# Kernel tuning notes

Measured on AMD Instinct MI355X. Metric: run time of the kernel, lower is better.

## Reference

```python
import jax, jax.numpy as jnp
import numpy as np

B, D, L, H, E = 65536, 3, 64, 256, 8
N_HIDDEN_EXTRA = 2  # num_hidden_layers - 1


def setup_inputs() -> dict:
    key = jax.random.key(0)
    ks = jax.random.split(key, 12)
    s = 0.05
    return {
        "x": jax.random.normal(ks[0], (B, D), jnp.float32),
        "labels": jax.random.randint(ks[1], (B,), 0, E, jnp.int64),
        "eps": jax.random.normal(ks[2], (B, L), jnp.float32),
        "mu_table": jax.random.normal(ks[3], (E, L), jnp.float32) * s,
        "logvar_table": jax.random.normal(ks[4], (E, L), jnp.float32) * s,
        "W0": jax.random.normal(ks[5], (E, D + L, H), jnp.float32) * s,
        "b0": jnp.zeros((E, H), jnp.float32),
        "Wh": jax.random.normal(ks[6], (N_HIDDEN_EXTRA, E, H, H), jnp.float32) * s,
        "bh": jnp.zeros((N_HIDDEN_EXTRA, E, H), jnp.float32),
        "Wo": jax.random.normal(ks[7], (E, H, 1), jnp.float32) * s,
        "bo": jnp.zeros((E, 1), jnp.float32),
    }


def reference(x, labels, eps, mu_table, logvar_table, W0, b0, Wh, bh, Wo, bo):
    batch = x.shape[0]
    # encoder: embedding lookup by label
    mu = mu_table[labels]          # [B, L]
    logvar = logvar_table[labels]  # [B, L]
    z = mu + eps * jnp.exp(0.5 * logvar)
    kl = -0.5 * jnp.sum(1.0 + logvar - mu * mu - jnp.exp(logvar)) / batch
    x_in = jnp.concatenate([x, z], axis=1)  # [B, D+L]
    # MoE dispatch: run each expert on the full batch, mask by label
    out = jnp.zeros((batch, 1), x.dtype)
    n_exp = W0.shape[0]
    n_hid = Wh.shape[0]
    for e in range(n_exp):
        h = jax.nn.relu(x_in @ W0[e] + b0[e])
        for l in range(n_hid):
            h = jax.nn.relu(h @ Wh[l, e] + bh[l, e])
        oe = h @ Wo[e] + bo[e]  # [B, 1]
        out = out + jnp.where((labels == e)[:, None], oe, 0.0)
    return out, kl
```

## Files before the change

kernel.cpp:

```cpp
#include <hip/hip_runtime.h>
#include <hip/hip_bf16.h>
#include <stdint.h>

#define B_N 65536
#define L_N 64
#define E_N 8
#define SPB 64
#define MAXT (B_N/SPB + E_N)
#define NHB 256
#define NPW 608
typedef __attribute__((ext_vector_type(4))) float f32x4;
typedef __attribute__((ext_vector_type(8))) short short8;

__device__ __forceinline__ short f2bf(float f){
  union { float f; unsigned u; } v; v.f = f;
  unsigned r = (v.u + 0x7fffu + ((v.u >> 16) & 1u)) >> 16;
  return (short)r;
}

__global__ void k_prep(const int* __restrict__ labels,
                       const float* __restrict__ W0, const float* __restrict__ Wh,
                       unsigned* __restrict__ pcnt,
                       short* __restrict__ wf0, short* __restrict__ wf1){
  const int bid = blockIdx.x, tid = threadIdx.x;
  if(bid < NHB){
    __shared__ unsigned lc[8];
    if(tid < 8) lc[tid] = 0;
    __syncthreads();
    atomicAdd(&lc[labels[bid*256 + tid] & 7], 1u);
    __syncthreads();
    if(tid < 8) pcnt[bid*8 + tid] = lc[tid];
    return;
  }
  int uid = (bid - NHB) * 256 + tid;
  const int NU0 = 8*3*16*64;
  const int NU1 = 2*8*8*16*64;
  if(uid < NU0){
    int e = uid / 3072, r = uid % 3072;
    int s = r / 1024, r2 = r % 1024, t = r2 / 64, l = r2 % 64;
    int g = l >> 4, m = 16*t + (l & 15);
    short8 v;
    #pragma unroll
    for(int j=0;j<8;j++){
      int k = 32*s + 4*g + (j & 3) + 16*(j >> 2);
      float f = (k < 67) ? W0[(e*67 + k)*256 + m] : 0.f;
      v[j] = f2bf(f);
    }
    *(short8*)(wf0 + (size_t)uid * 8) = v;
  } else if(uid < NU0 + NU1){
    int u = uid - NU0;
    int lh = u / 65536, r = u % 65536;
    int e = r / 8192, r1 = r % 8192;
    int s = r1 / 1024, r2 = r1 % 1024, t = r2 / 64, l = r2 % 64;
    int g = l >> 4, m = 16*t + (l & 15);
    short8 v;
    #pragma unroll
    for(int j=0;j<8;j++){
      int k = 32*s + 4*g + (j & 3) + 16*(j >> 2);
      v[j] = f2bf(Wh[(((size_t)(lh*8 + e))*256 + k)*256 + m]);
    }
    *(short8*)(wf1 + (size_t)u * 8) = v;
  }
}

__global__ void k_scan(const unsigned* __restrict__ pcnt,
                       unsigned* __restrict__ sbase,
                       int* __restrict__ te, int* __restrict__ tb, int* __restrict__ tl,
                       const float* __restrict__ mu_t, const float* __restrict__ lv_t,
                       float* __restrict__ klout){
  __shared__ unsigned spc[NHB*8];
  __shared__ int off[9], ts[9];
  __shared__ unsigned cnt[8];
  __shared__ float fe[8];
  const int t = threadIdx.x;
  for(int i=t; i<NHB*8; i+=256) spc[i] = pcnt[i];
  __syncthreads();
  if(t < 8){
    unsigned run = 0;
    for(int b=0;b<NHB;b++){ unsigned v = spc[b*8+t]; spc[b*8+t] = run; run += v; }
    cnt[t] = run;
    float s = 0.f;
    for(int i=0;i<64;i++){
      float m = mu_t[t*64+i], l = lv_t[t*64+i];
      s += 1.f + l - m*m - expf(l);
    }
    fe[t] = s;
  }
  __syncthreads();
  if(t == 0){
    int o = 0, tt = 0;
    for(int e=0;e<8;e++){
      off[e] = o; ts[e] = tt;
      o += (int)cnt[e];
      tt += ((int)cnt[e] + SPB - 1) / SPB;
    }
    off[8] = o; ts[8] = tt;
    float kl = 0.f;
    for(int e=0;e<8;e++) kl += fe[e] * (float)cnt[e];
    klout[0] = -0.5f * kl / (float)B_N;
  }
  __syncthreads();
  for(int i=t; i<NHB*8; i+=256) sbase[i] = (unsigned)off[i & 7] + spc[i];
  for(int i=t; i<MAXT; i+=256){
    if(i < ts[8]){
      int e = 0;
      while(e < 7 && i >= ts[e+1]) e++;
      te[i] = e;
      tb[i] = off[e] + (i - ts[e]) * SPB;
      tl[i] = off[e] + (int)cnt[e];
    } else { te[i] = 0; tb[i] = 0; tl[i] = 0; }
  }
}

__global__ void k_scatter(const int* __restrict__ labels,
                          const unsigned* __restrict__ sbase,
                          int* __restrict__ perm){
  __shared__ unsigned lcnt[8];
  const int bid = blockIdx.x, tid = threadIdx.x;
  if(tid < 8) lcnt[tid] = 0;
  __syncthreads();
  int i = bid*256 + tid;
  int e = labels[i] & 7;
  unsigned r = atomicAdd(&lcnt[e], 1u);
  perm[sbase[bid*8 + e] + r] = i;
}

__global__ __launch_bounds__(256, 2) void k_mlp(
    const float* __restrict__ x, const float* __restrict__ eps,
    const float* __restrict__ mu_t, const float* __restrict__ lv_t,
    const float* __restrict__ b0, const float* __restrict__ bh,
    const float* __restrict__ Wo, const float* __restrict__ bo,
    const short* __restrict__ wf0, const short* __restrict__ wf1,
    const int* __restrict__ perm, const int* __restrict__ te,
    const int* __restrict__ tb, const int* __restrict__ tl,
    float* __restrict__ out)
{
  __shared__ __align__(16) short abuf[3][8192];
  __shared__ __align__(16) float bias_lds[3][256];
  __shared__ __align__(16) float wo_lds[256];

  const int tid  = threadIdx.x;
  const int w    = tid >> 6, lane = tid & 63;
  const int g    = lane >> 4, col = lane & 15;
  const int bid  = blockIdx.x;
  const int e = te[bid], base = tb[bid], lim = tl[bid];
  if(base >= lim) return;

  bias_lds[0][tid] = b0[e*256 + tid];
  bias_lds[1][tid] = bh[e*256 + tid];
  bias_lds[2][tid] = bh[(8 + e)*256 + tid];
  wo_lds[tid]      = Wo[e*256 + tid];

  const int pos = base + w*16 + col;
  const bool valid = pos < lim;
  const int sid = perm[valid ? pos : (lim - 1)];
  const float bo_e = bo[e];

  short8 bx[3];
  #pragma unroll
  for(int s=0;s<3;s++){
    short8 v;
    #pragma unroll
    for(int jh=0;jh<2;jh++){
      #pragma unroll
      for(int q=0;q<4;q++){
        int k = 32*s + 4*g + 16*jh + q;
        float f = 0.f;
        if(k < 3) f = x[sid*3 + k];
        else if(k < 67){
          int zi = k - 3;
          f = mu_t[e*64 + zi] + eps[(size_t)sid*64 + zi] * __expf(0.5f * lv_t[e*64 + zi]);
        }
        v[jh*4 + q] = f2bf(f);
      }
    }
    bx[s] = v;
  }

  const short* w0e = wf0 + (size_t)e * (3*8192);
  const short* w1e = wf1 + (size_t)(0*8 + e) * (8*8192);
  const short* w2e = wf1 + (size_t)(1*8 + e) * (8*8192);

  f32x4 acc[16];
  #pragma unroll
  for(int t=0;t<16;t++) acc[t] = (f32x4){0.f,0.f,0.f,0.f};
  short8 hb[8];

  auto stage = [&](const short* srcT, int bufidx){
    #pragma unroll
    for(int c=0;c<4;c++){
      const char* gp = (const char*)srcT + c*4096 + tid*16;
      char* lp = (char*)&abuf[bufidx][0] + c*4096 + w*1024;
      __builtin_amdgcn_global_load_lds((const __attribute__((address_space(1))) void*)gp,
                                       (__attribute__((address_space(3))) void*)lp, 16, 0, 0);
    }
  };

  auto compute = [&](int bufidx, short8 b){
    const char* ab = (const char*)&abuf[bufidx][0];
    __builtin_amdgcn_s_setprio(1);
    #pragma unroll
    for(int t=0;t<16;t++){
      short8 a = *(const short8*)(ab + t*1024 + lane*16);
      acc[t] = __builtin_amdgcn_mfma_f32_16x16x32_bf16(a, b, acc[t], 0, 0, 0);
    }
    __builtin_amdgcn_s_setprio(0);
  };

  auto epilogue = [&](const float* bias_row){
    #pragma unroll
    for(int t=0;t<16;t++){
      f32x4 b4 = *(const f32x4*)(bias_row + 16*t + 4*g);
      #pragma unroll
      for(int r=0;r<4;r++){
        float vv = acc[t][r] + b4[r];
        acc[t][r] = vv > 0.f ? vv : 0.f;
      }
    }
    #pragma unroll
    for(int s=0;s<8;s++){
      short8 h;
      #pragma unroll
      for(int r=0;r<4;r++){ h[r] = f2bf(acc[2*s][r]); h[4+r] = f2bf(acc[2*s+1][r]); }
      hb[s] = h;
    }
    #pragma unroll
    for(int t=0;t<16;t++) acc[t] = (f32x4){0.f,0.f,0.f,0.f};
  };

  #define SRC_OF(u) ((u) < 3 ? (w0e + (u)*8192) : (u) < 11 ? (w1e + ((u)-3)*8192) \
                             : (w2e + ((u)-11)*8192))
  #define DO_TILE(T, H)                                                           \
    { if((T) < 17){ asm volatile("s_waitcnt vmcnt(4) lgkmcnt(0)" ::: "memory"); } \
      else        { asm volatile("s_waitcnt vmcnt(0) lgkmcnt(0)" ::: "memory"); } \
      __builtin_amdgcn_s_barrier();                                               \
      if((T) + 2 < 19) stage(SRC_OF((T)+2 < 19 ? (T)+2 : 18), ((T)+2) % 3);       \
      compute((T) % 3, H); }

  stage(SRC_OF(0), 0);
  stage(SRC_OF(1), 1);

  DO_TILE(0, bx[0])
  DO_TILE(1, bx[1])
  DO_TILE(2, bx[2])
  epilogue(&bias_lds[0][0]);

  DO_TILE(3,  hb[0])
  DO_TILE(4,  hb[1])
  DO_TILE(5,  hb[2])
  DO_TILE(6,  hb[3])
  DO_TILE(7,  hb[4])
  DO_TILE(8,  hb[5])
  DO_TILE(9,  hb[6])
  DO_TILE(10, hb[7])
  epilogue(&bias_lds[1][0]);

  DO_TILE(11, hb[0])
  DO_TILE(12, hb[1])
  DO_TILE(13, hb[2])
  DO_TILE(14, hb[3])
  DO_TILE(15, hb[4])
  DO_TILE(16, hb[5])
  DO_TILE(17, hb[6])
  DO_TILE(18, hb[7])
  #undef DO_TILE
  #undef SRC_OF

  float dot = 0.f;
  #pragma unroll
  for(int t=0;t<16;t++){
    f32x4 b4 = *(const f32x4*)(&bias_lds[2][16*t + 4*g]);
    f32x4 w4 = *(const f32x4*)(&wo_lds[16*t + 4*g]);
    #pragma unroll
    for(int r=0;r<4;r++){
      float vv = acc[t][r] + b4[r];
      vv = vv > 0.f ? vv : 0.f;
      dot += vv * w4[r];
    }
  }
  dot += __shfl_xor(dot, 16, 64);
  dot += __shfl_xor(dot, 32, 64);
  if(g == 0 && valid) out[sid] = dot + bo_e;
}

extern "C" void kernel_launch(void* const* d_in, const int* in_sizes, int n_in,
                              void* d_out, int out_size, void* d_ws, size_t ws_size,
                              hipStream_t stream){
  (void)in_sizes; (void)n_in; (void)out_size; (void)ws_size;
  const float* x   = (const float*)d_in[0];
  const int*   lab = (const int*)d_in[1];
  const float* eps = (const float*)d_in[2];
  const float* mu  = (const float*)d_in[3];
  const float* lv  = (const float*)d_in[4];
  const float* W0  = (const float*)d_in[5];
  const float* b0  = (const float*)d_in[6];
  const float* Wh  = (const float*)d_in[7];
  const float* bh  = (const float*)d_in[8];
  const float* Wo  = (const float*)d_in[9];
  const float* bo  = (const float*)d_in[10];
  float* out = (float*)d_out;

  char* ws = (char*)d_ws;
  unsigned* pcnt  = (unsigned*)(ws + 128);
  unsigned* sbase = (unsigned*)(ws + 8448);
  int* te   = (int*)(ws + 16640);
  int* tb   = (int*)(ws + 16640 + 4*MAXT);
  int* tl   = (int*)(ws + 16640 + 8*MAXT);
  int* perm = (int*)(ws + 32768);
  short* wf0 = (short*)(ws + 294912);
  short* wf1 = (short*)(ws + 688128);

  k_prep<<<NHB + NPW, 256, 0, stream>>>(lab, W0, Wh, pcnt, wf0, wf1);
  k_scan<<<1, 256, 0, stream>>>(pcnt, sbase, te, tb, tl, mu, lv, out + B_N);
  k_scatter<<<NHB, 256, 0, stream>>>(lab, sbase, perm);
  k_mlp<<<MAXT, 256, 0, stream>>>(x, eps, mu, lv, b0, bh, Wo, bo,
                                  wf0, wf1, perm, te, tb, tl, out);
}
```

Measured before the change: 56.47 us.

## Process two sample sub-tiles per wave to reuse each staged weight tile

Doubles samples per block from 64 to 128, so each wave computes two 16-sample column groups that share every A-fragment read from LDS. Each staged weight tile now feeds twice as many MFMAs, which halves weight traffic per sample and the number of blocks. The cost is doubled accumulator and activation registers, which may lower occupancy or cause spills, and fewer blocks when per-expert tail tiles are partly empty.

```diff
diff --git a/kernel.cpp b/kernel.cpp
--- a/kernel.cpp
+++ b/kernel.cpp
@@ -5,7 +5,7 @@
 #define B_N 65536
 #define L_N 64
 #define E_N 8
-#define SPB 64
+#define SPB 128
 #define MAXT (B_N/SPB + E_N)
 #define NHB 256
 #define NPW 608
@@ -151,40 +151,44 @@
   bias_lds[2][tid] = bh[(8 + e)*256 + tid];
   wo_lds[tid]      = Wo[e*256 + tid];
 
-  const int pos = base + w*16 + col;
-  const bool valid = pos < lim;
-  const int sid = perm[valid ? pos : (lim - 1)];
+  const int pos0 = base + w*32 + col;
+  const int pos1 = pos0 + 16;
+  const bool v0 = pos0 < lim, v1 = pos1 < lim;
+  const int sid0 = perm[v0 ? pos0 : (lim - 1)];
+  const int sid1 = perm[v1 ? pos1 : (lim - 1)];
   const float bo_e = bo[e];
 
-  short8 bx[3];
+  short8 hb0[8], hb1[8];
   #pragma unroll
   for(int s=0;s<3;s++){
-    short8 v;
+    short8 va, vb;
     #pragma unroll
     for(int jh=0;jh<2;jh++){
       #pragma unroll
       for(int q=0;q<4;q++){
         int k = 32*s + 4*g + 16*jh + q;
-        float f = 0.f;
-        if(k < 3) f = x[sid*3 + k];
+        float fa = 0.f, fb = 0.f;
+        if(k < 3){ fa = x[sid0*3 + k]; fb = x[sid1*3 + k]; }
         else if(k < 67){
           int zi = k - 3;
-          f = mu_t[e*64 + zi] + eps[(size_t)sid*64 + zi] * __expf(0.5f * lv_t[e*64 + zi]);
+          float m = mu_t[e*64 + zi], sd = __expf(0.5f * lv_t[e*64 + zi]);
+          fa = m + eps[(size_t)sid0*64 + zi] * sd;
+          fb = m + eps[(size_t)sid1*64 + zi] * sd;
         }
-        v[jh*4 + q] = f2bf(f);
+        va[jh*4 + q] = f2bf(fa);
+        vb[jh*4 + q] = f2bf(fb);
       }
     }
-    bx[s] = v;
+    hb0[s] = va; hb1[s] = vb;
   }
 
   const short* w0e = wf0 + (size_t)e * (3*8192);
   const short* w1e = wf1 + (size_t)(0*8 + e) * (8*8192);
   const short* w2e = wf1 + (size_t)(1*8 + e) * (8*8192);
 
-  f32x4 acc[16];
+  f32x4 acc0[16], acc1[16];
   #pragma unroll
-  for(int t=0;t<16;t++) acc[t] = (f32x4){0.f,0.f,0.f,0.f};
-  short8 hb[8];
+  for(int t=0;t<16;t++){ acc0[t] = (f32x4){0.f,0.f,0.f,0.f}; acc1[t] = (f32x4){0.f,0.f,0.f,0.f}; }
 
   auto stage = [&](const short* srcT, int bufidx){
     #pragma unroll
@@ -196,18 +200,19 @@
     }
   };
 
-  auto compute = [&](int bufidx, short8 b){
+  auto compute = [&](int bufidx, short8 b0f, short8 b1f){
     const char* ab = (const char*)&abuf[bufidx][0];
     __builtin_amdgcn_s_setprio(1);
     #pragma unroll
     for(int t=0;t<16;t++){
       short8 a = *(const short8*)(ab + t*1024 + lane*16);
-      acc[t] = __builtin_amdgcn_mfma_f32_16x16x32_bf16(a, b, acc[t], 0, 0, 0);
+      acc0[t] = __builtin_amdgcn_mfma_f32_16x16x32_bf16(a, b0f, acc0[t], 0, 0, 0);
+      acc1[t] = __builtin_amdgcn_mfma_f32_16x16x32_bf16(a, b1f, acc1[t], 0, 0, 0);
     }
     __builtin_amdgcn_s_setprio(0);
   };
 
-  auto epilogue = [&](const float* bias_row){
+  auto epi_set = [&](f32x4* acc, short8* hb, const float* bias_row){
     #pragma unroll
     for(int t=0;t<16;t++){
       f32x4 b4 = *(const f32x4*)(bias_row + 16*t + 4*g);
@@ -230,57 +235,63 @@
 
   #define SRC_OF(u) ((u) < 3 ? (w0e + (u)*8192) : (u) < 11 ? (w1e + ((u)-3)*8192) \
                              : (w2e + ((u)-11)*8192))
-  #define DO_TILE(T, H)                                                           \
+  #define DO_TILE(T, H0, H1)                                                      \
     { if((T) < 17){ asm volatile("s_waitcnt vmcnt(4) lgkmcnt(0)" ::: "memory"); } \
       else        { asm volatile("s_waitcnt vmcnt(0) lgkmcnt(0)" ::: "memory"); } \
       __builtin_amdgcn_s_barrier();                                               \
       if((T) + 2 < 19) stage(SRC_OF((T)+2 < 19 ? (T)+2 : 18), ((T)+2) % 3);       \
-      compute((T) % 3, H); }
+      compute((T) % 3, H0, H1); }
 
   stage(SRC_OF(0), 0);
   stage(SRC_OF(1), 1);
 
-  DO_TILE(0, bx[0])
-  DO_TILE(1, bx[1])
-  DO_TILE(2, bx[2])
-  epilogue(&bias_lds[0][0]);
-
-  DO_TILE(3,  hb[0])
-  DO_TILE(4,  hb[1])
-  DO_TILE(5,  hb[2])
-  DO_TILE(6,  hb[3])
-  DO_TILE(7,  hb[4])
-  DO_TILE(8,  hb[5])
-  DO_TILE(9,  hb[6])
-  DO_TILE(10, hb[7])
-  epilogue(&bias_lds[1][0]);
-
-  DO_TILE(11, hb[0])
-  DO_TILE(12, hb[1])
-  DO_TILE(13, hb[2])
-  DO_TILE(14, hb[3])
-  DO_TILE(15, hb[4])
-  DO_TILE(16, hb[5])
-  DO_TILE(17, hb[6])
-  DO_TILE(18, hb[7])
+  DO_TILE(0, hb0[0], hb1[0])
+  DO_TILE(1, hb0[1], hb1[1])
+  DO_TILE(2, hb0[2], hb1[2])
+  epi_set(acc0, hb0, &bias_lds[0][0]);
+  epi_set(acc1, hb1, &bias_lds[0][0]);
+
+  DO_TILE(3,  hb0[0], hb1[0])
+  DO_TILE(4,  hb0[1], hb1[1])
+  DO_TILE(5,  hb0[2], hb1[2])
+  DO_TILE(6,  hb0[3], hb1[3])
+  DO_TILE(7,  hb0[4], hb1[4])
+  DO_TILE(8,  hb0[5], hb1[5])
+  DO_TILE(9,  hb0[6], hb1[6])
+  DO_TILE(10, hb0[7], hb1[7])
+  epi_set(acc0, hb0, &bias_lds[1][0]);
+  epi_set(acc1, hb1, &bias_lds[1][0]);
+
+  DO_TILE(11, hb0[0], hb1[0])
+  DO_TILE(12, hb0[1], hb1[1])
+  DO_TILE(13, hb0[2], hb1[2])
+  DO_TILE(14, hb0[3], hb1[3])
+  DO_TILE(15, hb0[4], hb1[4])
+  DO_TILE(16, hb0[5], hb1[5])
+  DO_TILE(17, hb0[6], hb1[6])
+  DO_TILE(18, hb0[7], hb1[7])
   #undef DO_TILE
   #undef SRC_OF
 
-  float dot = 0.f;
+  float d0 = 0.f, d1 = 0.f;
   #pragma unroll
   for(int t=0;t<16;t++){
     f32x4 b4 = *(const f32x4*)(&bias_lds[2][16*t + 4*g]);
     f32x4 w4 = *(const f32x4*)(&wo_lds[16*t + 4*g]);
     #pragma unroll
     for(int r=0;r<4;r++){
-      float vv = acc[t][r] + b4[r];
-      vv = vv > 0.f ? vv : 0.f;
-      dot += vv * w4[r];
-    }
-  }
-  dot += __shfl_xor(dot, 16, 64);
-  dot += __shfl_xor(dot, 32, 64);
-  if(g == 0 && valid) out[sid] = dot + bo_e;
+      float u0 = acc0[t][r] + b4[r]; u0 = u0 > 0.f ? u0 : 0.f;
+      float u1 = acc1[t][r] + b4[r]; u1 = u1 > 0.f ? u1 : 0.f;
+      d0 += u0 * w4[r];
+      d1 += u1 * w4[r];
+    }
+  }
+  d0 += __shfl_xor(d0, 16, 64);
+  d0 += __shfl_xor(d0, 32, 64);
+  d1 += __shfl_xor(d1, 16, 64);
+  d1 += __shfl_xor(d1, 32, 64);
+  if(g == 0 && v0) out[sid0] = d0 + bo_e;
+  if(g == 0 && v1) out[sid1] = d1 + bo_e;
 }
 
 extern "C" void kernel_launch(void* const* d_in, const int* in_sizes, int n_in,
```

Result: slower. 64.41 us (+14.1%).
